# Optimization experiments

Hardware: AMD Instinct MI355X
Metric: run time of the kernel (lower is better)

## Reference

```python
import jax, jax.numpy as jnp
import numpy as np

B, T, C = 4, 2048, 1024
H, Dh = 16, 64
EPS = 1e-5

def _layernorm(x, g, b):
    mu = jnp.mean(x, axis=-1, keepdims=True)
    var = jnp.mean(jnp.square(x - mu), axis=-1, keepdims=True)
    return (x - mu) * jax.lax.rsqrt(var + EPS) * g + b

def setup_inputs() -> dict:
    key = jax.random.key(0)
    ks = jax.random.split(key, 12)
    s = lambda fan_in: 1.0 / np.sqrt(fan_in)
    return {
        "x":  jax.random.normal(ks[0], (B, T, C), dtype=jnp.float32),
        "Wq": jax.random.uniform(ks[1], (C, H * Dh), jnp.float32, -s(C), s(C)),
        "Wk": jax.random.uniform(ks[2], (C, H * Dh), jnp.float32, -s(C), s(C)),
        "Wv": jax.random.uniform(ks[3], (C, H * Dh), jnp.float32, -s(C), s(C)),
        "Wo": jax.random.uniform(ks[4], (H * Dh, C), jnp.float32, -s(H * Dh), s(H * Dh)),
        "bo": jnp.zeros((C,), jnp.float32),
        "W1": jax.random.uniform(ks[5], (C, 4 * C), jnp.float32, -s(C), s(C)),
        "b1": jnp.zeros((4 * C,), jnp.float32),
        "W2": jax.random.uniform(ks[6], (4 * C, C), jnp.float32, -s(4 * C), s(4 * C)),
        "b2": jnp.zeros((C,), jnp.float32),
        "g1": jnp.ones((C,), jnp.float32),
        "be1": jnp.zeros((C,), jnp.float32),
        "g2": jnp.ones((C,), jnp.float32),
        "be2": jnp.zeros((C,), jnp.float32),
    }

def reference(x, Wq, Wk, Wv, Wo, bo, W1, b1, W2, b2, g1, be1, g2, be2):
    # --- pre-LN attention ---
    h = _layernorm(x, g1, be1)                                   # [B,T,C]
    q = (h @ Wq).reshape(B, T, H, Dh)                            # per-head projections fused
    k = (h @ Wk).reshape(B, T, H, Dh)
    v = (h @ Wv).reshape(B, T, H, Dh)
    scores = jnp.einsum('bqhd,bkhd->bhqk', q, k) * (Dh ** -0.5)  # [B,H,T,T]
    causal = jnp.tril(jnp.ones((T, T), dtype=bool))
    scores = jnp.where(causal, scores, -jnp.inf)
    wei = jax.nn.softmax(scores, axis=-1)                        # dropout p=0 (eval)
    attn = jnp.einsum('bhqk,bkhd->bqhd', wei, v).reshape(B, T, H * Dh)
    x = x + attn @ Wo + bo
    # --- pre-LN MLP ---
    h2 = _layernorm(x, g2, be2)
    x = x + jax.nn.relu(h2 @ W1 + b1) @ W2 + b2
    return x
```

## Files before the change

### kernel.cpp

```cpp
#include <hip/hip_runtime.h>
#include <hip/hip_bf16.h>

typedef __hip_bfloat16 bf16;
typedef __attribute__((ext_vector_type(8))) short short8;
typedef __attribute__((ext_vector_type(4))) short s16x4;
typedef __attribute__((ext_vector_type(4))) float f32x4;

__device__ __forceinline__ float s2f(short s) {
    unsigned u = ((unsigned)(unsigned short)s) << 16;
    return __builtin_bit_cast(float, u);
}
__device__ __forceinline__ short f2s(float f) {
    bf16 h = __float2bfloat16(f);
    return __builtin_bit_cast(short, h);
}
__device__ __forceinline__ void gload_lds16(const void* g, void* l) {
    __builtin_amdgcn_global_load_lds(
        (const __attribute__((address_space(1))) unsigned int*)g,
        (__attribute__((address_space(3))) unsigned int*)l, 16, 0, 0);
}

#define PH_VM8  asm volatile("s_waitcnt vmcnt(8)" ::: "memory")
#define PH_VM4  asm volatile("s_waitcnt vmcnt(4)" ::: "memory")
#define PH_VM0  asm volatile("s_waitcnt vmcnt(0)" ::: "memory")
#define PH_BAR  __builtin_amdgcn_s_barrier()
#define PH_LGKM do { asm volatile("s_waitcnt lgkmcnt(0)" ::: "memory"); \
                     __builtin_amdgcn_sched_barrier(0); } while (0)

__global__ __launch_bounds__(256) void tconv_kernel(const float* __restrict__ src,
                                                    short* __restrict__ dst,
                                                    int R, int C) {
    __shared__ short tile[64][65];
    const int r0 = blockIdx.y * 64, c0 = blockIdx.x * 64;
    const int t = threadIdx.x;
    const int lr = t >> 2, lc = (t & 3) * 16;
    const float* sp = src + (size_t)(r0 + lr) * C + c0 + lc;
#pragma unroll
    for (int q = 0; q < 4; q++) {
        f32x4 v = *(const f32x4*)(const void*)(sp + q * 4);
#pragma unroll
        for (int j = 0; j < 4; j++) tile[lr][lc + q * 4 + j] = f2s(v[j]);
    }
    __syncthreads();
    short8 o0, o1;
#pragma unroll
    for (int j = 0; j < 8; j++) { o0[j] = tile[lc + j][lr]; o1[j] = tile[lc + 8 + j][lr]; }
    short* dp = dst + (size_t)(c0 + lr) * R + r0 + lc;
    *(short8*)(void*)dp = o0;
    *(short8*)(void*)(dp + 8) = o1;
}

__global__ __launch_bounds__(256) void ln_kernel(const float* __restrict__ x,
                                                 const float* __restrict__ g,
                                                 const float* __restrict__ beta,
                                                 bf16* __restrict__ out) {
    const int t = threadIdx.x;
    const int w = t >> 6, lane = t & 63;
    const int row = blockIdx.x * 4 + w;
    const float* xr = x + (size_t)row * 1024;
    float v[16];
    float s = 0.f, ss = 0.f;
#pragma unroll
    for (int p = 0; p < 4; p++) {
        f32x4 xv = *(const f32x4*)(const void*)(xr + p * 256 + lane * 4);
#pragma unroll
        for (int j = 0; j < 4; j++) {
            v[p * 4 + j] = xv[j];
            s += xv[j];
            ss += xv[j] * xv[j];
        }
    }
#pragma unroll
    for (int off = 32; off >= 1; off >>= 1) {
        s += __shfl_xor(s, off);
        ss += __shfl_xor(ss, off);
    }
    const float mu = s * (1.0f / 1024.0f);
    const float var = ss * (1.0f / 1024.0f) - mu * mu;
    const float rstd = rsqrtf(var + 1e-5f);
    short* orow = (short*)(void*)(out + (size_t)row * 1024);
#pragma unroll
    for (int p = 0; p < 4; p++) {
        const int c = p * 256 + lane * 4;
        f32x4 gv = *(const f32x4*)(const void*)(g + c);
        f32x4 bv = *(const f32x4*)(const void*)(beta + c);
        s16x4 o;
#pragma unroll
        for (int j = 0; j < 4; j++)
            o[j] = f2s((v[p * 4 + j] - mu) * rstd * gv[j] + bv[j]);
        *(s16x4*)(void*)(orow + c) = o;
    }
}

__global__ __launch_bounds__(256) void gemm64(const bf16* __restrict__ A,
                                              const bf16* __restrict__ Bt,
                                              const float* __restrict__ bias,
                                              const float* resid,
                                              void* Cp, int c_f32,
                                              int m_base, int N, int K,
                                              int relu_flag) {
    __shared__ short As[64 * 64];
    __shared__ short Bs[64 * 64];

    const int t = threadIdx.x;
    const int m0 = blockIdx.x * 64;
    const int n0 = blockIdx.y * 64;
    const int w = t >> 6;
    const int lane = t & 63;
    const int wm = (w >> 1) * 32;
    const int wn = (w & 1) * 32;

    const int sr = t >> 2, sk = (t & 3) * 8;
    const bf16* aA = A + (size_t)(m0 + sr) * K + sk;
    const bf16* aB = Bt + (size_t)(n0 + sr) * K + sk;
    short* ldsA0 = &As[w * 512];
    short* ldsA1 = &As[2048 + w * 512];
    short* ldsB0 = &Bs[w * 512];
    short* ldsB1 = &Bs[2048 + w * 512];

    const int l = lane & 15;
    const int lk = (lane >> 4) * 8;

    f32x4 acc[2][2] = {};

    for (int k0 = 0; k0 < K; k0 += 64) {
        __syncthreads();
        gload_lds16(aA + k0, ldsA0);
        gload_lds16(aA + k0 + 32, ldsA1);
        gload_lds16(aB + k0, ldsB0);
        gload_lds16(aB + k0 + 32, ldsB1);
        __syncthreads();
#pragma unroll
        for (int ks = 0; ks < 2; ks++) {
            short8 a0 = *(const short8*)&As[ks * 2048 + (wm + l) * 32 + lk];
            short8 a1 = *(const short8*)&As[ks * 2048 + (wm + 16 + l) * 32 + lk];
            short8 b0 = *(const short8*)&Bs[ks * 2048 + (wn + l) * 32 + lk];
            short8 b1 = *(const short8*)&Bs[ks * 2048 + (wn + 16 + l) * 32 + lk];
            acc[0][0] = __builtin_amdgcn_mfma_f32_16x16x32_bf16(a0, b0, acc[0][0], 0, 0, 0);
            acc[0][1] = __builtin_amdgcn_mfma_f32_16x16x32_bf16(a0, b1, acc[0][1], 0, 0, 0);
            acc[1][0] = __builtin_amdgcn_mfma_f32_16x16x32_bf16(a1, b0, acc[1][0], 0, 0, 0);
            acc[1][1] = __builtin_amdgcn_mfma_f32_16x16x32_bf16(a1, b1, acc[1][1], 0, 0, 0);
        }
    }

    const int lrow4 = (lane >> 4) * 4;
#pragma unroll
    for (int mi = 0; mi < 2; mi++)
#pragma unroll
        for (int r = 0; r < 4; r++) {
            const int grow = m_base + m0 + wm + mi * 16 + lrow4 + r;
#pragma unroll
            for (int ni = 0; ni < 2; ni++) {
                const int gcol = n0 + wn + ni * 16 + l;
                float val = acc[mi][ni][r];
                if (bias) val += bias[gcol];
                if (relu_flag) val = fmaxf(val, 0.f);
                const size_t ci = (size_t)grow * N + gcol;
                if (resid) val += resid[ci];
                if (c_f32) ((float*)Cp)[ci] = val;
                else        ((short*)Cp)[ci] = f2s(val);
            }
        }
}

#define MM_BLOCK(ACC)                                                        \
    do {                                                                     \
        __builtin_amdgcn_s_setprio(1);                                       \
        _Pragma("unroll")                                                    \
        for (int mi_ = 0; mi_ < 4; mi_++)                                    \
            _Pragma("unroll")                                                \
            for (int ni_ = 0; ni_ < 4; ni_++)                                \
                ACC[mi_][ni_] = __builtin_amdgcn_mfma_f32_16x16x32_bf16(     \
                    af[mi_], bf[ni_], ACC[mi_][ni_], 0, 0, 0);               \
        __builtin_amdgcn_s_setprio(0);                                       \
    } while (0)

__global__ __launch_bounds__(512, 2) void gemm256(const bf16* __restrict__ A,
                                                  const bf16* __restrict__ Bt,
                                                  const float* __restrict__ bias,
                                                  bf16* __restrict__ Cp,
                                                  int N, int relu_flag) {
    __shared__ char lds[131072];
    constexpr int NT = 16;

    const int t = threadIdx.x;
    const int w = t >> 6, lane = t & 63;
    const int l = lane & 15, g = lane >> 4;
    const int m0 = blockIdx.x * 256, n0 = blockIdx.y * 256;
    const int wm = (w >> 2) * 128, wn = (w & 3) * 64;
    const int qx = (g ^ ((l >> 1) & 3)) * 16;
    const int qh8 = (((lane & 3) ^ ((lane >> 3) & 3)) * 8);
    const int srow = w * 32 + (lane >> 2);
    const short* Asrc = (const short*)A;
    const short* Bsrc = (const short*)Bt;

    f32x4 accL[4][4] = {};
    f32x4 accH[4][4] = {};
    short8 af[4], bf[4];

    auto stage = [&](int th, int j) {
        const int ks = j >> 1, mat = j & 1;
        char* slot = lds + ((th & 1) << 16) + (mat << 15) + (ks << 14);
        const short* mp = mat ? Bsrc : Asrc;
        const int rowb = (mat ? n0 : m0);
        const int kc = th * 64 + ks * 32 + qh8;
        gload_lds16(mp + (size_t)(rowb + srow) * 1024 + kc,      slot + (w * 2) * 1024);
        gload_lds16(mp + (size_t)(rowb + srow + 16) * 1024 + kc, slot + (w * 2 + 1) * 1024);
    };
    auto lda = [&](const char* rb, int mi, int ks) -> short8 {
        return *(const short8*)(rb + (ks << 14) + (wm + mi * 16 + l) * 64 + qx);
    };
    auto ldb = [&](const char* rb, int ni, int ks) -> short8 {
        return *(const short8*)(rb + 32768 + (ks << 14) + (wn + ni * 16 + l) * 64 + qx);
    };

    stage(0, 0); stage(0, 1); stage(0, 2); stage(0, 3); stage(1, 0); stage(1, 1);

    for (int it = 0; it < NT - 1; ++it) {
        const char* rb = lds + ((it & 1) << 16);
        PH_VM8; PH_BAR;
#pragma unroll
        for (int i = 0; i < 4; i++) af[i] = lda(rb, i, 0);
#pragma unroll
        for (int i = 0; i < 4; i++) bf[i] = ldb(rb, i, 0);
        stage(it + 1, 2);
        PH_LGKM;
        MM_BLOCK(accL);
#pragma unroll
        for (int i = 0; i < 4; i++) af[i] = lda(rb, 4 + i, 0);
        stage(it + 1, 3);
        PH_BAR; PH_LGKM;
        MM_BLOCK(accH);
        PH_VM8; PH_BAR;
#pragma unroll
        for (int i = 0; i < 4; i++) af[i] = lda(rb, i, 1);
#pragma unroll
        for (int i = 0; i < 4; i++) bf[i] = ldb(rb, i, 1);
        if (it + 2 < NT) stage(it + 2, 0);
        PH_LGKM;
        MM_BLOCK(accL);
#pragma unroll
        for (int i = 0; i < 4; i++) af[i] = lda(rb, 4 + i, 1);
        if (it + 2 < NT) stage(it + 2, 1);
        PH_BAR; PH_LGKM;
        MM_BLOCK(accH);
    }
    {
        const char* rb = lds + (((NT - 1) & 1) << 16);
        PH_VM4; PH_BAR;
#pragma unroll
        for (int i = 0; i < 4; i++) af[i] = lda(rb, i, 0);
#pragma unroll
        for (int i = 0; i < 4; i++) bf[i] = ldb(rb, i, 0);
        PH_LGKM;
        MM_BLOCK(accL);
#pragma unroll
        for (int i = 0; i < 4; i++) af[i] = lda(rb, 4 + i, 0);
        PH_BAR; PH_LGKM;
        MM_BLOCK(accH);
        PH_VM0; PH_BAR;
#pragma unroll
        for (int i = 0; i < 4; i++) af[i] = lda(rb, i, 1);
#pragma unroll
        for (int i = 0; i < 4; i++) bf[i] = ldb(rb, i, 1);
        PH_LGKM;
        MM_BLOCK(accL);
#pragma unroll
        for (int i = 0; i < 4; i++) af[i] = lda(rb, 4 + i, 1);
        PH_BAR; PH_LGKM;
        MM_BLOCK(accH);
    }

#pragma unroll
    for (int half = 0; half < 2; half++)
#pragma unroll
        for (int mi = 0; mi < 4; mi++)
#pragma unroll
            for (int r = 0; r < 4; r++) {
                const int grow = m0 + wm + (half * 4 + mi) * 16 + g * 4 + r;
                short* crow = (short*)(void*)Cp + (size_t)grow * N;
#pragma unroll
                for (int ni = 0; ni < 4; ni++) {
                    const int gcol = n0 + wn + ni * 16 + l;
                    float val = half ? accH[mi][ni][r] : accL[mi][ni][r];
                    if (bias) val += bias[gcol];
                    if (relu_flag) val = fmaxf(val, 0.f);
                    crow[gcol] = f2s(val);
                }
            }
}

__global__ __launch_bounds__(256) void attn_kernel(const bf16* __restrict__ qkv,
                                                   bf16* __restrict__ o) {
    __shared__ short KsF[64 * 64];
    __shared__ short Vt[64][72];
    __shared__ short Pl[4][32][72];

    const int bh = blockIdx.x;
    const int b = bh >> 4, h = bh & 15;
    const int qt = 15 - blockIdx.y;
    const int q0 = qt * 128;
    const size_t rbase = (size_t)b * 2048;
    const int hcol = h * 64;

    const int t = threadIdx.x;
    const int w = t >> 6;
    const int lane = t & 63;
    const int l = lane & 15;
    const int g = lane >> 4;
    const int sp = t >> 3;
    const int sb = (t & 7) * 8;

    const int qw0 = q0 + 32 * w;
    short8 qf[2][2];
#pragma unroll
    for (int mi = 0; mi < 2; mi++)
#pragma unroll
        for (int ks = 0; ks < 2; ks++) {
            const short* qp = (const short*)qkv +
                (rbase + qw0 + mi * 16 + l) * 3072 + hcol + ks * 32 + g * 8;
            short8 tv = *(const short8*)(const void*)qp;
            short8 sv;
#pragma unroll
            for (int e = 0; e < 8; e++) sv[e] = f2s(s2f(tv[e]) * 0.125f);
            qf[mi][ks] = sv;
        }

    const int key_a = w * 16 + (lane >> 3);
    const int kd = (lane & 7) ^ ((lane >> 3) & 7);
    const short* kgA = (const short*)qkv + (rbase + key_a) * 3072 + 1024 + hcol + kd * 8;
    const short* kgB = kgA + 8 * 3072;
    short* kdstA = &KsF[w * 1024];
    short* kdstB = &KsF[w * 1024 + 512];

    f32x4 o_acc[2][4] = {};
    f32x4 l_acc[2] = {};
    short8 onesf;
    {
        const short ov = (l == 0) ? (short)0x3F80 : (short)0;
#pragma unroll
        for (int e = 0; e < 8; e++) onesf[e] = ov;
    }
    const f32x4 s_init = {-12.f, -12.f, -12.f, -12.f};

    const int kt_max = (q0 + 127) >> 6;
    for (int kt = 0; kt <= kt_max; kt++) {
        const int k0 = kt * 64;
        const short* vg = (const short*)qkv + (rbase + k0 + 2 * sp) * 3072 + 2048 + hcol + sb;
        short8 vv0 = *(const short8*)(const void*)vg;
        short8 vv1 = *(const short8*)(const void*)(vg + 3072);
        __syncthreads();
        gload_lds16(kgA + (size_t)k0 * 3072, kdstA);
        gload_lds16(kgB + (size_t)k0 * 3072, kdstB);
        {
            const int key = 2 * sp;
            const int cbk = key >> 3;
            const int kin = key & 7;
#pragma unroll
            for (int j = 0; j < 8; j++) {
                const int d = sb + j;
                const int col = ((cbk ^ (d >> 3)) << 3) + kin;
                int pk = (int)(unsigned short)vv0[j] | ((int)(unsigned short)vv1[j] << 16);
                *(int*)(void*)&Vt[d][col] = pk;
            }
        }
        __syncthreads();

        if (k0 <= qw0 + 31) {
            const bool needMask = (k0 + 63 > qw0);
            f32x4 s_acc[2][4];
#pragma unroll
            for (int mi = 0; mi < 2; mi++)
#pragma unroll
                for (int ni = 0; ni < 4; ni++) s_acc[mi][ni] = s_init;
#pragma unroll
            for (int ks = 0; ks < 2; ks++) {
                short8 kf[4];
#pragma unroll
                for (int ni = 0; ni < 4; ni++) {
                    const int key = ni * 16 + l;
                    const int c = key * 8 + ((ks * 4 + g) ^ (key & 7));
                    kf[ni] = *(const short8*)&KsF[c * 8];
                }
#pragma unroll
                for (int mi = 0; mi < 2; mi++)
#pragma unroll
                    for (int ni = 0; ni < 4; ni++)
                        s_acc[mi][ni] = __builtin_amdgcn_mfma_f32_16x16x32_bf16(
                            qf[mi][ks], kf[ni], s_acc[mi][ni], 0, 0, 0);
            }
#pragma unroll
            for (int mi = 0; mi < 2; mi++)
#pragma unroll
                for (int r = 0; r < 4; r++) {
                    const int qg = qw0 + mi * 16 + 4 * g + r;
#pragma unroll
                    for (int ni = 0; ni < 4; ni++) {
                        float s = s_acc[mi][ni][r];
                        if (needMask && (k0 + ni * 16 + l > qg)) s = -1e30f;
                        Pl[w][mi * 16 + 4 * g + r][ni * 16 + l] = f2s(__expf(s));
                    }
                }
#pragma unroll
            for (int ks = 0; ks < 2; ks++) {
                short8 pf[2], vf[4];
#pragma unroll
                for (int mi = 0; mi < 2; mi++)
                    pf[mi] = *(const short8*)&Pl[w][mi * 16 + l][ks * 32 + g * 8];
#pragma unroll
                for (int nd = 0; nd < 4; nd++) {
                    const int d = nd * 16 + l;
                    const int cb = ks * 4 + g;
                    vf[nd] = *(const short8*)&Vt[d][((cb ^ (d >> 3)) << 3)];
                }
#pragma unroll
                for (int mi = 0; mi < 2; mi++) {
                    l_acc[mi] = __builtin_amdgcn_mfma_f32_16x16x32_bf16(
                        pf[mi], onesf, l_acc[mi], 0, 0, 0);
#pragma unroll
                    for (int nd = 0; nd < 4; nd++)
                        o_acc[mi][nd] = __builtin_amdgcn_mfma_f32_16x16x32_bf16(
                            pf[mi], vf[nd], o_acc[mi][nd], 0, 0, 0);
                }
            }
        }
    }

#pragma unroll
    for (int mi = 0; mi < 2; mi++)
#pragma unroll
        for (int r = 0; r < 4; r++) {
            float lsum = __shfl(l_acc[mi][r], lane & 48);
            const float inv = 1.0f / lsum;
            const int qg = qw0 + mi * 16 + 4 * g + r;
            short* op = (short*)(void*)(o + (rbase + qg) * 1024 + hcol);
#pragma unroll
            for (int nd = 0; nd < 4; nd++)
                op[nd * 16 + l] = f2s(o_acc[mi][nd][r] * inv);
        }
}

extern "C" void kernel_launch(void* const* d_in, const int* in_sizes, int n_in,
                              void* d_out, int out_size, void* d_ws, size_t ws_size,
                              hipStream_t stream) {
    const float* x   = (const float*)d_in[0];
    const float* Wq  = (const float*)d_in[1];
    const float* Wk  = (const float*)d_in[2];
    const float* Wv  = (const float*)d_in[3];
    const float* Wo  = (const float*)d_in[4];
    const float* bo  = (const float*)d_in[5];
    const float* W1  = (const float*)d_in[6];
    const float* b1  = (const float*)d_in[7];
    const float* W2  = (const float*)d_in[8];
    const float* b2  = (const float*)d_in[9];
    const float* g1  = (const float*)d_in[10];
    const float* be1 = (const float*)d_in[11];
    const float* g2  = (const float*)d_in[12];
    const float* be2 = (const float*)d_in[13];

    char* ws = (char*)d_ws;
    const size_t MB = (size_t)1024 * 1024;
    bf16*  s0  = (bf16*)(ws);
    bf16*  qkv = (bf16*)(ws + 16 * MB);
    short* WoT = (short*)(ws + 16 * MB);
    short* W1T = (short*)(ws);
    short* W2T = (short*)(ws + 8 * MB);
    bf16*  h2  = (bf16*)(ws + 16 * MB);
    bf16*  m1  = (bf16*)(ws + 32 * MB);
    short* WT  = (short*)d_out;
    float* x1  = (float*)d_out;

    const int M = 8192, C = 1024, F = 4096, MH = 4096;

    tconv_kernel<<<dim3(16, 16), 256, 0, stream>>>(Wq, WT,                   C, C);
    tconv_kernel<<<dim3(16, 16), 256, 0, stream>>>(Wk, WT + 1024 * 1024,     C, C);
    tconv_kernel<<<dim3(16, 16), 256, 0, stream>>>(Wv, WT + 2 * 1024 * 1024, C, C);

    ln_kernel<<<M / 4, 256, 0, stream>>>(x, g1, be1, s0);

    gemm256<<<dim3(M / 256, 3072 / 256), 512, 0, stream>>>(
        s0, (const bf16*)WT, nullptr, qkv, 3072, 0);

    attn_kernel<<<dim3(64, 16), 256, 0, stream>>>(qkv, s0);

    tconv_kernel<<<dim3(16, 16), 256, 0, stream>>>(Wo, WoT, C, C);
    gemm64<<<dim3(M / 64, C / 64), 256, 0, stream>>>(
        s0, (const bf16*)WoT, bo, x, x1, 1, 0, C, C, 0);

    tconv_kernel<<<dim3(64, 16), 256, 0, stream>>>(W1, W1T, C, F);
    tconv_kernel<<<dim3(16, 64), 256, 0, stream>>>(W2, W2T, F, C);

    ln_kernel<<<M / 4, 256, 0, stream>>>(x1, g2, be2, h2);

    for (int half = 0; half < 2; half++) {
        const bf16* Ah = h2 + (size_t)half * MH * C;
        gemm256<<<dim3(MH / 256, F / 256), 512, 0, stream>>>(
            Ah, (const bf16*)W1T, b1, m1, F, 1);
        gemm64<<<dim3(MH / 64, C / 64), 256, 0, stream>>>(
            m1, (const bf16*)W2T, b2, x1, d_out, 1, half * MH, C, F, 0);
    }
}
```

Before: 544.1 us.

## Use split-K gemm256 with atomics for W2, add block swizzle, exp2 softmax

The MLP down-projection now uses the 256x256 MFMA gemm instead of gemm64. K is split four ways and fp32 partial sums are atomically added into the output buffer, which already holds the residual x1. gemm256 also remaps workgroup IDs with a swizzle meant to improve L2 locality. The attention softmax folds log2(e) into the Q scale and the initial score offset, so it can use exp2f instead of __expf. The cost is many fp32 atomic adds to global memory and a summation order that is no longer deterministic.

Measured after the change: 667.3 us. 1.23x slower.

```diff
diff --git a/kernel.cpp b/kernel.cpp
--- a/kernel.cpp
+++ b/kernel.cpp
@@ -178,15 +178,27 @@
 __global__ __launch_bounds__(512, 2) void gemm256(const bf16* __restrict__ A,
                                                   const bf16* __restrict__ Bt,
                                                   const float* __restrict__ bias,
-                                                  bf16* __restrict__ Cp,
-                                                  int N, int relu_flag) {
+                                                  void* Cp,
+                                                  int N, int ldk, int nbn,
+                                                  int m_base, int c_atomic,
+                                                  int relu_flag) {
     __shared__ char lds[131072];
     constexpr int NT = 16;
 
     const int t = threadIdx.x;
     const int w = t >> 6, lane = t & 63;
     const int l = lane & 15, g = lane >> 4;
-    const int m0 = blockIdx.x * 256, n0 = blockIdx.y * 256;
+
+    const int nwg = gridDim.x * gridDim.y;
+    const int orig = blockIdx.y * gridDim.x + blockIdx.x;
+    const int swz = (orig & 7) * (nwg >> 3) + (orig >> 3);
+    const int bm = swz % gridDim.x;
+    const int byy = swz / gridDim.x;
+    const int bn = byy % nbn;
+    const int split = byy / nbn;
+
+    const int m0 = bm * 256, n0 = bn * 256;
+    const int kbase = split << 10;
     const int wm = (w >> 2) * 128, wn = (w & 3) * 64;
     const int qx = (g ^ ((l >> 1) & 3)) * 16;
     const int qh8 = (((lane & 3) ^ ((lane >> 3) & 3)) * 8);
@@ -203,9 +215,9 @@
         char* slot = lds + ((th & 1) << 16) + (mat << 15) + (ks << 14);
         const short* mp = mat ? Bsrc : Asrc;
         const int rowb = (mat ? n0 : m0);
-        const int kc = th * 64 + ks * 32 + qh8;
-        gload_lds16(mp + (size_t)(rowb + srow) * 1024 + kc,      slot + (w * 2) * 1024);
-        gload_lds16(mp + (size_t)(rowb + srow + 16) * 1024 + kc, slot + (w * 2 + 1) * 1024);
+        const int kc = kbase + th * 64 + ks * 32 + qh8;
+        gload_lds16(mp + (size_t)(rowb + srow) * ldk + kc,      slot + (w * 2) * 1024);
+        gload_lds16(mp + (size_t)(rowb + srow + 16) * ldk + kc, slot + (w * 2 + 1) * 1024);
     };
     auto lda = [&](const char* rb, int mi, int ks) -> short8 {
         return *(const short8*)(rb + (ks << 14) + (wm + mi * 16 + l) * 64 + qx);
@@ -271,21 +283,23 @@
         MM_BLOCK(accH);
     }
 
+    const bool addb = (bias != nullptr) && (split == 0);
 #pragma unroll
     for (int half = 0; half < 2; half++)
 #pragma unroll
         for (int mi = 0; mi < 4; mi++)
 #pragma unroll
             for (int r = 0; r < 4; r++) {
-                const int grow = m0 + wm + (half * 4 + mi) * 16 + g * 4 + r;
-                short* crow = (short*)(void*)Cp + (size_t)grow * N;
+                const int grow = m_base + m0 + wm + (half * 4 + mi) * 16 + g * 4 + r;
+                const size_t rowoff = (size_t)grow * N;
 #pragma unroll
                 for (int ni = 0; ni < 4; ni++) {
                     const int gcol = n0 + wn + ni * 16 + l;
                     float val = half ? accH[mi][ni][r] : accL[mi][ni][r];
-                    if (bias) val += bias[gcol];
+                    if (addb) val += bias[gcol];
                     if (relu_flag) val = fmaxf(val, 0.f);
-                    crow[gcol] = f2s(val);
+                    if (c_atomic) atomicAdd((float*)Cp + rowoff + gcol, val);
+                    else ((short*)Cp)[rowoff + gcol] = f2s(val);
                 }
             }
 }
@@ -322,7 +336,7 @@
             short8 tv = *(const short8*)(const void*)qp;
             short8 sv;
 #pragma unroll
-            for (int e = 0; e < 8; e++) sv[e] = f2s(s2f(tv[e]) * 0.125f);
+            for (int e = 0; e < 8; e++) sv[e] = f2s(s2f(tv[e]) * 0.18033688f);
             qf[mi][ks] = sv;
         }
 
@@ -341,7 +355,7 @@
 #pragma unroll
         for (int e = 0; e < 8; e++) onesf[e] = ov;
     }
-    const f32x4 s_init = {-12.f, -12.f, -12.f, -12.f};
+    const f32x4 s_init = {-17.3123405f, -17.3123405f, -17.3123405f, -17.3123405f};
 
     const int kt_max = (q0 + 127) >> 6;
     for (int kt = 0; kt <= kt_max; kt++) {
@@ -398,7 +412,7 @@
                     for (int ni = 0; ni < 4; ni++) {
                         float s = s_acc[mi][ni][r];
                         if (needMask && (k0 + ni * 16 + l > qg)) s = -1e30f;
-                        Pl[w][mi * 16 + 4 * g + r][ni * 16 + l] = f2s(__expf(s));
+                        Pl[w][mi * 16 + 4 * g + r][ni * 16 + l] = f2s(exp2f(s));
                     }
                 }
 #pragma unroll
@@ -479,7 +493,7 @@
     ln_kernel<<<M / 4, 256, 0, stream>>>(x, g1, be1, s0);
 
     gemm256<<<dim3(M / 256, 3072 / 256), 512, 0, stream>>>(
-        s0, (const bf16*)WT, nullptr, qkv, 3072, 0);
+        s0, (const bf16*)WT, nullptr, qkv, 3072, 1024, 12, 0, 0, 0);
 
     attn_kernel<<<dim3(64, 16), 256, 0, stream>>>(qkv, s0);
 
@@ -495,8 +509,8 @@
     for (int half = 0; half < 2; half++) {
         const bf16* Ah = h2 + (size_t)half * MH * C;
         gemm256<<<dim3(MH / 256, F / 256), 512, 0, stream>>>(
-            Ah, (const bf16*)W1T, b1, m1, F, 1);
-        gemm64<<<dim3(MH / 64, C / 64), 256, 0, stream>>>(
-            m1, (const bf16*)W2T, b2, x1, d_out, 1, half * MH, C, F, 0);
-    }
-}
+            Ah, (const bf16*)W1T, b1, m1, 4096, 1024, 16, 0, 0, 1);
+        gemm256<<<dim3(MH / 256, 16), 512, 0, stream>>>(
+            m1, (const bf16*)W2T, b2, d_out, 1024, 4096, 4, half * MH, 1, 0);
+    }
+}
```
